# Performance work log

Hardware: AMD Instinct MI355X
Metric: run time of the kernel (lower is better)

Reference implementation:

```python
import jax, jax.numpy as jnp
import numpy as np

N, T, INPUT_DIM, HIDDEN_DIM = 8, 4096, 128, 128


def setup_inputs() -> dict:
    key = jax.random.key(0)
    k_h, k_wq, k_bq, k_wk, k_bk = jax.random.split(key, 5)
    s = 1.0 / np.sqrt(INPUT_DIM)
    return {
        "H": jax.random.normal(k_h, (N, T, INPUT_DIM), dtype=jnp.float32),
        "Wq": jax.random.uniform(k_wq, (INPUT_DIM, HIDDEN_DIM), jnp.float32, -s, s),
        "bq": jax.random.uniform(k_bq, (HIDDEN_DIM,), jnp.float32, -s, s),
        "Wk": jax.random.uniform(k_wk, (INPUT_DIM, HIDDEN_DIM), jnp.float32, -s, s),
        "bk": jax.random.uniform(k_bk, (HIDDEN_DIM,), jnp.float32, -s, s),
    }


def reference(H, Wq, bq, Wk, bk):
    # Q, K: [N, T, hidden]
    Q = jnp.einsum("ntd,dh->nth", H, Wq) + bq
    K = jnp.einsum("ntd,dh->nth", H, Wk) + bk
    # Faithful quirk: original scales by sqrt(K.transpose(-1,-2).size(-1)) == sqrt(T),
    # NOT sqrt(hidden_dim).
    T_ = H.shape[1]
    scale = 1.0 / jnp.sqrt(jnp.asarray(T_, dtype=H.dtype))
    A = jnp.einsum("nth,nsh->nts", Q, K) * scale  # [N, T, T]
    A = jax.nn.softmax(A, axis=-1)
    # Attention applied directly to H (no V projection), plus residual.
    return jnp.einsum("nts,nsd->ntd", A, H) + H
```

## Files before the change

### kernel.cpp

```cpp
#include <hip/hip_runtime.h>
#include <hip/hip_bf16.h>

typedef __attribute__((ext_vector_type(4))) float f32x4;
typedef __attribute__((ext_vector_type(16))) float f32x16;
typedef __attribute__((ext_vector_type(8))) short s16x8;
typedef unsigned int u32;

#define DEVINL static __device__ __forceinline__

constexpr int TDIM = 4096;
constexpr int DDIM = 128;
constexpr float QSCALE = 1.4426950408889634f / 64.0f;

DEVINL unsigned short f2bf(float f) {
  union { float f; unsigned u; } v; v.f = f;
  unsigned r = v.u + 0x7fffu + ((v.u >> 16) & 1u);
  return (unsigned short)(r >> 16);
}

__global__ void wtrans_kernel(const float* __restrict__ Wq,
                              const float* __restrict__ Wk,
                              unsigned short* __restrict__ Wtq,
                              unsigned short* __restrict__ Wtk) {
  const float* src = blockIdx.x ? Wk : Wq;
  unsigned short* dst = blockIdx.x ? Wtk : Wtq;
  int tid = threadIdx.x;
  for (int k = 0; k < 64; ++k) {
    int e = tid + k * 256;
    int h = e >> 7, d = e & 127;
    dst[h * 128 + d] = f2bf(src[d * 128 + h]);
  }
}

__global__ __launch_bounds__(256) void proj_kernel(
    const float* __restrict__ H, const float* __restrict__ bq,
    const float* __restrict__ bk, const unsigned short* __restrict__ Wtq,
    const unsigned short* __restrict__ Wtk, char* __restrict__ Qb,
    char* __restrict__ Kb, char* __restrict__ Vt) {
  __shared__ __align__(16) unsigned short hs[64][136];
  __shared__ __align__(16) char qs[16384];
  __shared__ __align__(16) char kt[16384];
  __shared__ __align__(16) char vt[16384];
  int b = blockIdx.x;
  int n = b >> 6;
  int t0 = (b & 63) << 6;
  int tid = threadIdx.x;
  const float* Hrow = H + (size_t)(n * TDIM + t0) * DDIM;
#pragma unroll
  for (int k = 0; k < 8; ++k) {
    int e = tid + k * 256;
    int r = e >> 5;
    int c = (e & 31) << 2;
    f32x4 v = *(const f32x4*)(Hrow + r * DDIM + c);
    unsigned short bf[4] = {f2bf(v.x), f2bf(v.y), f2bf(v.z), f2bf(v.w)};
    unsigned short* p = &hs[r][c];
    p[0] = bf[0]; p[1] = bf[1]; p[2] = bf[2]; p[3] = bf[3];
#pragma unroll
    for (int j = 0; j < 4; ++j) {
      int d = c + j;
      int byte = ((d >> 1) * 256 + (d & 1) * 128 + r * 2) ^
                 (((d >> 1) & 15) << 4);
      *(unsigned short*)(vt + byte) = bf[j];
    }
  }
  __syncthreads();
  int w = tid >> 6, ln = tid & 63;
  int lm = ln & 15, lg = ln >> 4;
  int m0 = w * 16;
  s16x8 af[4];
#pragma unroll
  for (int kf = 0; kf < 4; ++kf)
    af[kf] = *(const s16x8*)&hs[m0 + lm][kf * 32 + lg * 8];
#pragma unroll
  for (int nt = 0; nt < 8; ++nt) {
    f32x4 acc = {0.f, 0.f, 0.f, 0.f};
#pragma unroll
    for (int kf = 0; kf < 4; ++kf) {
      s16x8 bfr = *(const s16x8*)&Wtq[(nt * 16 + lm) * 128 + kf * 32 + lg * 8];
      acc = __builtin_amdgcn_mfma_f32_16x16x32_bf16(af[kf], bfr, acc, 0, 0, 0);
    }
    int h = nt * 16 + lm;
    float bv = bq[h];
#pragma unroll
    for (int i = 0; i < 4; ++i) {
      int tl = m0 + lg * 4 + i;
      int byte = tl * 256 + ((h * 2) ^ ((tl & 15) << 4));
      *(unsigned short*)(qs + byte) = f2bf((acc[i] + bv) * QSCALE);
    }
  }
#pragma unroll
  for (int nt = 0; nt < 8; ++nt) {
    f32x4 acc = {0.f, 0.f, 0.f, 0.f};
#pragma unroll
    for (int kf = 0; kf < 4; ++kf) {
      s16x8 bfr = *(const s16x8*)&Wtk[(nt * 16 + lm) * 128 + kf * 32 + lg * 8];
      acc = __builtin_amdgcn_mfma_f32_16x16x32_bf16(af[kf], bfr, acc, 0, 0, 0);
    }
    int hip2 = ((lm >> 3) & 1) * 32;
    int jj = lm & 7;
#pragma unroll
    for (int i = 0; i < 4; ++i) {
      int rl = m0 + lg * 4 + i;
      int byte = (rl >> 5) * 8192 + nt * 1024 + (hip2 + (rl & 31)) * 16 + jj * 2;
      *(unsigned short*)(kt + byte) = f2bf(acc[i] + bk[nt * 16 + lm]);
    }
  }
  __syncthreads();
  size_t base = (size_t)(n * TDIM + t0) * 256;
  size_t vbase = ((size_t)(n * 64 + (t0 >> 6)) << 14);
#pragma unroll
  for (int k = 0; k < 4; ++k) {
    int off = tid * 16 + k * 4096;
    *(f32x4*)(Qb + base + off) = *(const f32x4*)(qs + off);
    *(f32x4*)(Kb + base + off) = *(const f32x4*)(kt + off);
    *(f32x4*)(Vt + vbase + off) = *(const f32x4*)(vt + off);
  }
}

DEVINL void stage16(const char* g, char* s, int w, int ln) {
#pragma unroll
  for (int j = 0; j < 2; ++j) {
    int off = (w * 2 + j) * 1024;
    __builtin_amdgcn_global_load_lds(
        (const __attribute__((address_space(1))) void*)(g + off + ln * 16),
        (__attribute__((address_space(3))) void*)(s + off), 16, 0, 0);
  }
}

__global__ __launch_bounds__(512, 2) void attn_kernel(
    const char* __restrict__ Qsw, const char* __restrict__ Ksw,
    const char* __restrict__ Vsw, const float* __restrict__ H,
    float* __restrict__ Out) {
  __shared__ __align__(16) char lds[69632];
  int b = blockIdx.x;
  int n = b & 7;
  int q0 = (b >> 3) << 7;
  int tid = threadIdx.x;
  int w = tid >> 6, ln = tid & 63;
  int q32 = ln & 31, hi = ln >> 5;
  int ws = w & 3;
  int st = w >> 2;
  int qrow = q0 + ws * 32;
  int swz = (q32 & 15) << 4;
  int dpl = q32 >> 1;
  int vswz = dpl << 4;
  int dphalf = (q32 & 1) * 128;

  const char* Kn = Ksw + (size_t)n * (TDIM * 256);
  const char* Vn0 = Vsw + (size_t)n * (64 * 16384);
  const char* Vn1 = Vn0 + (size_t)32 * 16384;

  const char* Qn = Qsw + (size_t)(n * TDIM + qrow + q32) * 256;
  s16x8 qf[8];
#pragma unroll
  for (int d = 0; d < 8; ++d)
    qf[d] = *(const s16x8*)(Qn + ((d * 32 + hi * 16) ^ swz));

  f32x16 o[4];
#pragma unroll
  for (int dt = 0; dt < 4; ++dt) o[dt] = (f32x16)0.0f;
  float lsum = 0.f;

  stage16(Vn0, lds + 0, w, ln);
  stage16(Vn1, lds + 32768, w, ln);
  __syncthreads();

  for (int it = 0; it < 32; ++it) {
    int c = it & 1;
    if (it < 31) {
      int p2 = c ^ 1;
      size_t go = (size_t)(it + 1) * 16384;
      stage16(Vn0 + go, lds + p2 * 16384, w, ln);
      stage16(Vn1 + go, lds + 32768 + p2 * 16384, w, ln);
    }
    const char* vb = lds + st * 32768 + c * 16384;
    const char* kt = Kn + ((size_t)(st * 32 + it) << 14);

    f32x16 s0 = (f32x16)0.0f, s1 = (f32x16)0.0f;
#pragma unroll
    for (int d = 0; d < 8; ++d) {
      s16x8 ka0 = *(const s16x8*)(kt + d * 1024 + ln * 16);
      s16x8 ka1 = *(const s16x8*)(kt + 8192 + d * 1024 + ln * 16);
      s0 = __builtin_amdgcn_mfma_f32_32x32x16_bf16(ka0, qf[d], s0, 0, 0, 0);
      s1 = __builtin_amdgcn_mfma_f32_32x32x16_bf16(ka1, qf[d], s1, 0, 0, 0);
    }

    f32x16 p0, p1;
#pragma unroll
    for (int r = 0; r < 16; ++r) {
      p0[r] = __builtin_amdgcn_exp2f(s0[r]);
      p1[r] = __builtin_amdgcn_exp2f(s1[r]);
    }
    float ls = 0.f;
#pragma unroll
    for (int r = 0; r < 16; ++r) ls += p0[r] + p1[r];
    lsum += ls;

    s16x8 pa[4];
#pragma unroll
    for (int kt2 = 0; kt2 < 2; ++kt2) {
      u32 P2[8];
#pragma unroll
      for (int r = 0; r < 8; ++r) {
        float e0 = kt2 ? p1[2 * r] : p0[2 * r];
        float e1 = kt2 ? p1[2 * r + 1] : p0[2 * r + 1];
        asm("v_cvt_pk_bf16_f32 %0, %1, %2" : "=v"(P2[r]) : "v"(e0), "v"(e1));
      }
#pragma unroll
      for (int b2 = 0; b2 < 2; ++b2) {
        u32 a0 = P2[b2 * 4 + 0], c0 = P2[b2 * 4 + 2];
        u32 a1 = P2[b2 * 4 + 1], c1 = P2[b2 * 4 + 3];
        asm("v_permlane32_swap_b32 %0, %1" : "+v"(a0), "+v"(c0));
        asm("v_permlane32_swap_b32 %0, %1" : "+v"(a1), "+v"(c1));
        union { u32 u[4]; s16x8 v; } pk;
        pk.u[0] = a0; pk.u[1] = a1; pk.u[2] = c0; pk.u[3] = c1;
        pa[kt2 * 2 + b2] = pk.v;
      }
    }

    __builtin_amdgcn_s_setprio(1);
#pragma unroll
    for (int ks = 0; ks < 4; ++ks) {
      int colv = dphalf + ks * 32 + hi * 16;
#pragma unroll
      for (int dt = 0; dt < 4; ++dt) {
        int dp = dt * 16 + dpl;
        s16x8 vv = *(const s16x8*)(vb + ((dp * 256 + colv) ^ vswz));
        o[dt] = __builtin_amdgcn_mfma_f32_32x32x16_bf16(pa[ks], vv, o[dt], 0, 0, 0);
      }
    }
    __builtin_amdgcn_s_setprio(0);
    __syncthreads();
  }

  if (w >= 4) {
    char* dst = lds + (w - 4) * 16896;
#pragma unroll
    for (int dt = 0; dt < 4; ++dt)
#pragma unroll
      for (int c4 = 0; c4 < 4; ++c4) {
        f32x4 ch = {o[dt][c4 * 4 + 0], o[dt][c4 * 4 + 1],
                    o[dt][c4 * 4 + 2], o[dt][c4 * 4 + 3]};
        *(f32x4*)(dst + ((dt * 4 + c4) * 64 + ln) * 16) = ch;
      }
    *(float*)(dst + 16384 + ln * 4) = lsum;
  }
  __syncthreads();
  if (w < 4) {
    const char* src = lds + w * 16896;
#pragma unroll
    for (int dt = 0; dt < 4; ++dt)
#pragma unroll
      for (int c4 = 0; c4 < 4; ++c4) {
        f32x4 ch = *(const f32x4*)(src + ((dt * 4 + c4) * 64 + ln) * 16);
        o[dt][c4 * 4 + 0] += ch.x; o[dt][c4 * 4 + 1] += ch.y;
        o[dt][c4 * 4 + 2] += ch.z; o[dt][c4 * 4 + 3] += ch.w;
      }
    lsum += *(const float*)(src + 16384 + ln * 4);
    u32 la = __builtin_bit_cast(u32, lsum), lb = la;
    asm("v_permlane32_swap_b32 %0, %1" : "+v"(la), "+v"(lb));
    float ltot = __builtin_bit_cast(float, la) + __builtin_bit_cast(float, lb);
    float invl = 1.0f / ltot;
    if (hi == 0) *(float*)(lds + 67584 + w * 128 + q32 * 4) = invl;
  }
  __syncthreads();
  if (w < 4) {
    const float* Hn = H + (size_t)n * TDIM * DDIM;
    float* On = Out + (size_t)n * TDIM * DDIM;
    float iv[16];
#pragma unroll
    for (int r = 0; r < 16; ++r) {
      int qr = (r & 3) + 8 * (r >> 2) + 4 * hi;
      iv[r] = *(const float*)(lds + 67584 + w * 128 + qr * 4);
    }
#pragma unroll
    for (int dt = 0; dt < 4; ++dt)
#pragma unroll
      for (int r = 0; r < 16; ++r) {
        int qr = (r & 3) + 8 * (r >> 2) + 4 * hi;
        size_t idx = (size_t)(qrow + qr) * DDIM + dt * 32 + q32;
        On[idx] = o[dt][r] * iv[r] + Hn[idx];
      }
  }
}

extern "C" void kernel_launch(void* const* d_in, const int* in_sizes, int n_in,
                              void* d_out, int out_size, void* d_ws, size_t ws_size,
                              hipStream_t stream) {
  const float* H  = (const float*)d_in[0];
  const float* Wq = (const float*)d_in[1];
  const float* bq = (const float*)d_in[2];
  const float* Wk = (const float*)d_in[3];
  const float* bk = (const float*)d_in[4];
  float* Out = (float*)d_out;
  char* ws = (char*)d_ws;
  unsigned short* Wtq = (unsigned short*)(ws);
  unsigned short* Wtk = (unsigned short*)(ws + 32768);
  char* Qb = ws + 65536;
  char* Kb = ws + 65536 + 8388608;
  char* Vt = ws + 65536 + 2 * 8388608;

  wtrans_kernel<<<2, 256, 0, stream>>>(Wq, Wk, Wtq, Wtk);
  proj_kernel<<<512, 256, 0, stream>>>(H, bq, bk, Wtq, Wtk, Qb, Kb, Vt);
  attn_kernel<<<256, 512, 0, stream>>>(Qb, Kb, Vt, H, Out);
}
```

Measured before the change: 126.1 us.

## Fold Wk into query projection and reuse bf16 H as keys

Scores are rewritten as (H Wq Wk^T + bq Wk^T) H^T: a prep kernel forms M = Wq Wk^T and u = Wk bq, and the key projection is dropped, since the bk term is constant per row and cancels in softmax. The attention kernel then stages both K (the bf16 H itself) and V tiles into a larger double-buffered LDS. Each wave now computes 64 query rows against a quarter of the key range, sharing each K and V fragment across two MFMAs, and partial results are combined through an LDS tree reduction. This removes one projection GEMM and halves fragment loads per MFMA, at the cost of 128KB of LDS, which likely limits the kernel to one block per CU, and more register pressure.

```diff
diff --git a/kernel.cpp b/kernel.cpp
--- a/kernel.cpp
+++ b/kernel.cpp
@@ -18,24 +18,27 @@
   return (unsigned short)(r >> 16);
 }
 
-__global__ void wtrans_kernel(const float* __restrict__ Wq,
-                              const float* __restrict__ Wk,
-                              unsigned short* __restrict__ Wtq,
-                              unsigned short* __restrict__ Wtk) {
-  const float* src = blockIdx.x ? Wk : Wq;
-  unsigned short* dst = blockIdx.x ? Wtk : Wtq;
-  int tid = threadIdx.x;
-  for (int k = 0; k < 64; ++k) {
-    int e = tid + k * 256;
-    int h = e >> 7, d = e & 127;
-    dst[h * 128 + d] = f2bf(src[d * 128 + h]);
+__global__ __launch_bounds__(256) void prep_kernel(
+    const float* __restrict__ Wq, const float* __restrict__ Wk,
+    const float* __restrict__ bq, unsigned short* __restrict__ Mt,
+    float* __restrict__ u) {
+  int idx = blockIdx.x * 256 + threadIdx.x;
+  int e = idx >> 7, d = idx & 127;
+  float acc = 0.f;
+#pragma unroll 4
+  for (int h = 0; h < 128; ++h) acc += Wq[d * 128 + h] * Wk[e * 128 + h];
+  Mt[e * 128 + d] = f2bf(acc);
+  if (blockIdx.x == 0 && threadIdx.x < 128) {
+    float a = 0.f;
+#pragma unroll 4
+    for (int h = 0; h < 128; ++h) a += Wk[threadIdx.x * 128 + h] * bq[h];
+    u[threadIdx.x] = a;
   }
 }
 
 __global__ __launch_bounds__(256) void proj_kernel(
-    const float* __restrict__ H, const float* __restrict__ bq,
-    const float* __restrict__ bk, const unsigned short* __restrict__ Wtq,
-    const unsigned short* __restrict__ Wtk, char* __restrict__ Qb,
+    const float* __restrict__ H, const unsigned short* __restrict__ Mt,
+    const float* __restrict__ u, char* __restrict__ Qb,
     char* __restrict__ Kb, char* __restrict__ Vt) {
   __shared__ __align__(16) unsigned short hs[64][136];
   __shared__ __align__(16) char qs[16384];
@@ -55,11 +58,16 @@
     unsigned short bf[4] = {f2bf(v.x), f2bf(v.y), f2bf(v.z), f2bf(v.w)};
     unsigned short* p = &hs[r][c];
     p[0] = bf[0]; p[1] = bf[1]; p[2] = bf[2]; p[3] = bf[3];
+    int kbyte = r * 256 + ((c * 2) ^ ((r & 15) << 4));
+    unsigned short* kp = (unsigned short*)(kt + kbyte);
+    kp[0] = bf[0]; kp[1] = bf[1]; kp[2] = bf[2]; kp[3] = bf[3];
+    int p32 = r >> 5, tl = r & 31;
 #pragma unroll
     for (int j = 0; j < 4; ++j) {
       int d = c + j;
-      int byte = ((d >> 1) * 256 + (d & 1) * 128 + r * 2) ^
-                 (((d >> 1) & 15) << 4);
+      int dp = d >> 1, half = d & 1;
+      int byte = p32 * 8192 + dp * 128 +
+                 ((half * 64 + tl * 2) ^ ((dp & 7) << 4));
       *(unsigned short*)(vt + byte) = bf[j];
     }
   }
@@ -76,38 +84,21 @@
     f32x4 acc = {0.f, 0.f, 0.f, 0.f};
 #pragma unroll
     for (int kf = 0; kf < 4; ++kf) {
-      s16x8 bfr = *(const s16x8*)&Wtq[(nt * 16 + lm) * 128 + kf * 32 + lg * 8];
+      s16x8 bfr = *(const s16x8*)&Mt[(nt * 16 + lm) * 128 + kf * 32 + lg * 8];
       acc = __builtin_amdgcn_mfma_f32_16x16x32_bf16(af[kf], bfr, acc, 0, 0, 0);
     }
-    int h = nt * 16 + lm;
-    float bv = bq[h];
+    int e = nt * 16 + lm;
+    float bv = u[e];
 #pragma unroll
     for (int i = 0; i < 4; ++i) {
       int tl = m0 + lg * 4 + i;
-      int byte = tl * 256 + ((h * 2) ^ ((tl & 15) << 4));
+      int byte = tl * 256 + ((e * 2) ^ ((tl & 15) << 4));
       *(unsigned short*)(qs + byte) = f2bf((acc[i] + bv) * QSCALE);
     }
   }
-#pragma unroll
-  for (int nt = 0; nt < 8; ++nt) {
-    f32x4 acc = {0.f, 0.f, 0.f, 0.f};
-#pragma unroll
-    for (int kf = 0; kf < 4; ++kf) {
-      s16x8 bfr = *(const s16x8*)&Wtk[(nt * 16 + lm) * 128 + kf * 32 + lg * 8];
-      acc = __builtin_amdgcn_mfma_f32_16x16x32_bf16(af[kf], bfr, acc, 0, 0, 0);
-    }
-    int hip2 = ((lm >> 3) & 1) * 32;
-    int jj = lm & 7;
-#pragma unroll
-    for (int i = 0; i < 4; ++i) {
-      int rl = m0 + lg * 4 + i;
-      int byte = (rl >> 5) * 8192 + nt * 1024 + (hip2 + (rl & 31)) * 16 + jj * 2;
-      *(unsigned short*)(kt + byte) = f2bf(acc[i] + bk[nt * 16 + lm]);
-    }
-  }
   __syncthreads();
   size_t base = (size_t)(n * TDIM + t0) * 256;
-  size_t vbase = ((size_t)(n * 64 + (t0 >> 6)) << 14);
+  size_t vbase = (size_t)(n * 128 + (t0 >> 5)) * 8192;
 #pragma unroll
   for (int k = 0; k < 4; ++k) {
     int off = tid * 16 + k * 4096;
@@ -117,13 +108,12 @@
   }
 }
 
-DEVINL void stage16(const char* g, char* s, int w, int ln) {
-#pragma unroll
-  for (int j = 0; j < 2; ++j) {
-    int off = (w * 2 + j) * 1024;
+DEVINL void stage8(const char* g, char* s, int ln) {
+#pragma unroll
+  for (int j = 0; j < 8; ++j) {
     __builtin_amdgcn_global_load_lds(
-        (const __attribute__((address_space(1))) void*)(g + off + ln * 16),
-        (__attribute__((address_space(3))) void*)(s + off), 16, 0, 0);
+        (const __attribute__((address_space(1))) void*)(g + j * 1024 + ln * 16),
+        (__attribute__((address_space(3))) void*)(s + j * 1024), 16, 0, 0);
   }
 }
 
@@ -131,81 +121,82 @@
     const char* __restrict__ Qsw, const char* __restrict__ Ksw,
     const char* __restrict__ Vsw, const float* __restrict__ H,
     float* __restrict__ Out) {
-  __shared__ __align__(16) char lds[69632];
+  __shared__ __align__(16) char lds[131072];
   int b = blockIdx.x;
   int n = b & 7;
   int q0 = (b >> 3) << 7;
   int tid = threadIdx.x;
   int w = tid >> 6, ln = tid & 63;
   int q32 = ln & 31, hi = ln >> 5;
-  int ws = w & 3;
-  int st = w >> 2;
-  int qrow = q0 + ws * 32;
+  int qg = w >> 2;
+  int kvs = w & 3;
+  int qrow = q0 + qg * 64;
   int swz = (q32 & 15) << 4;
   int dpl = q32 >> 1;
-  int vswz = dpl << 4;
-  int dphalf = (q32 & 1) * 128;
+  int vcol = (q32 & 1) * 64;
 
   const char* Kn = Ksw + (size_t)n * (TDIM * 256);
-  const char* Vn0 = Vsw + (size_t)n * (64 * 16384);
-  const char* Vn1 = Vn0 + (size_t)32 * 16384;
-
-  const char* Qn = Qsw + (size_t)(n * TDIM + qrow + q32) * 256;
-  s16x8 qf[8];
-#pragma unroll
-  for (int d = 0; d < 8; ++d)
-    qf[d] = *(const s16x8*)(Qn + ((d * 32 + hi * 16) ^ swz));
-
-  f32x16 o[4];
-#pragma unroll
-  for (int dt = 0; dt < 4; ++dt) o[dt] = (f32x16)0.0f;
-  float lsum = 0.f;
-
-  stage16(Vn0, lds + 0, w, ln);
-  stage16(Vn1, lds + 32768, w, ln);
+  const char* Vn = Vsw + (size_t)n * (128 * 8192);
+
+  const char* Qlo = Qsw + (size_t)(n * TDIM + qrow + q32) * 256;
+  const char* Qhi = Qlo + 32 * 256;
+  s16x8 qfl[8], qfh[8];
+#pragma unroll
+  for (int d = 0; d < 8; ++d) {
+    int off = (d * 32 + hi * 16) ^ swz;
+    qfl[d] = *(const s16x8*)(Qlo + off);
+    qfh[d] = *(const s16x8*)(Qhi + off);
+  }
+
+  f32x16 o[8];
+#pragma unroll
+  for (int i = 0; i < 8; ++i) o[i] = (f32x16)0.0f;
+  float lsl = 0.f, lsh = 0.f;
+
+  int stp = w & 3, typ = w >> 2;
+  {
+    const char* g = typ ? (Vn + (size_t)(stp * 32) * 8192)
+                        : (Kn + (size_t)(stp * 1024) * 256);
+    stage8(g, lds + stp * 16384 + typ * 8192, ln);
+  }
   __syncthreads();
 
   for (int it = 0; it < 32; ++it) {
     int c = it & 1;
     if (it < 31) {
-      int p2 = c ^ 1;
-      size_t go = (size_t)(it + 1) * 16384;
-      stage16(Vn0 + go, lds + p2 * 16384, w, ln);
-      stage16(Vn1 + go, lds + 32768 + p2 * 16384, w, ln);
-    }
-    const char* vb = lds + st * 32768 + c * 16384;
-    const char* kt = Kn + ((size_t)(st * 32 + it) << 14);
-
-    f32x16 s0 = (f32x16)0.0f, s1 = (f32x16)0.0f;
+      int kvn = stp * 1024 + (it + 1) * 32;
+      const char* g = typ ? (Vn + (size_t)(kvn >> 5) * 8192)
+                          : (Kn + (size_t)kvn * 256);
+      stage8(g, lds + (c ^ 1) * 65536 + stp * 16384 + typ * 8192, ln);
+    }
+    const char* kb = lds + c * 65536 + kvs * 16384;
+    const char* vb = kb + 8192;
+
+    f32x16 sl = (f32x16)0.0f, sh = (f32x16)0.0f;
+    __builtin_amdgcn_s_setprio(1);
 #pragma unroll
     for (int d = 0; d < 8; ++d) {
-      s16x8 ka0 = *(const s16x8*)(kt + d * 1024 + ln * 16);
-      s16x8 ka1 = *(const s16x8*)(kt + 8192 + d * 1024 + ln * 16);
-      s0 = __builtin_amdgcn_mfma_f32_32x32x16_bf16(ka0, qf[d], s0, 0, 0, 0);
-      s1 = __builtin_amdgcn_mfma_f32_32x32x16_bf16(ka1, qf[d], s1, 0, 0, 0);
-    }
-
-    f32x16 p0, p1;
+      s16x8 ka = *(const s16x8*)(kb + (q32 * 256 + ((d * 32 + hi * 16) ^ swz)));
+      sl = __builtin_amdgcn_mfma_f32_32x32x16_bf16(ka, qfl[d], sl, 0, 0, 0);
+      sh = __builtin_amdgcn_mfma_f32_32x32x16_bf16(ka, qfh[d], sh, 0, 0, 0);
+    }
+    __builtin_amdgcn_s_setprio(0);
+
 #pragma unroll
     for (int r = 0; r < 16; ++r) {
-      p0[r] = __builtin_amdgcn_exp2f(s0[r]);
-      p1[r] = __builtin_amdgcn_exp2f(s1[r]);
-    }
-    float ls = 0.f;
-#pragma unroll
-    for (int r = 0; r < 16; ++r) ls += p0[r] + p1[r];
-    lsum += ls;
-
-    s16x8 pa[4];
-#pragma unroll
-    for (int kt2 = 0; kt2 < 2; ++kt2) {
+      sl[r] = __builtin_amdgcn_exp2f(sl[r]);
+      lsl += sl[r];
+      sh[r] = __builtin_amdgcn_exp2f(sh[r]);
+      lsh += sh[r];
+    }
+
+    s16x8 pal[2], pah[2];
+    {
       u32 P2[8];
 #pragma unroll
-      for (int r = 0; r < 8; ++r) {
-        float e0 = kt2 ? p1[2 * r] : p0[2 * r];
-        float e1 = kt2 ? p1[2 * r + 1] : p0[2 * r + 1];
-        asm("v_cvt_pk_bf16_f32 %0, %1, %2" : "=v"(P2[r]) : "v"(e0), "v"(e1));
-      }
+      for (int r = 0; r < 8; ++r)
+        asm("v_cvt_pk_bf16_f32 %0, %1, %2"
+            : "=v"(P2[r]) : "v"(sl[2 * r]), "v"(sl[2 * r + 1]));
 #pragma unroll
       for (int b2 = 0; b2 < 2; ++b2) {
         u32 a0 = P2[b2 * 4 + 0], c0 = P2[b2 * 4 + 2];
@@ -214,74 +205,96 @@
         asm("v_permlane32_swap_b32 %0, %1" : "+v"(a1), "+v"(c1));
         union { u32 u[4]; s16x8 v; } pk;
         pk.u[0] = a0; pk.u[1] = a1; pk.u[2] = c0; pk.u[3] = c1;
-        pa[kt2 * 2 + b2] = pk.v;
+        pal[b2] = pk.v;
+      }
+#pragma unroll
+      for (int r = 0; r < 8; ++r)
+        asm("v_cvt_pk_bf16_f32 %0, %1, %2"
+            : "=v"(P2[r]) : "v"(sh[2 * r]), "v"(sh[2 * r + 1]));
+#pragma unroll
+      for (int b2 = 0; b2 < 2; ++b2) {
+        u32 a0 = P2[b2 * 4 + 0], c0 = P2[b2 * 4 + 2];
+        u32 a1 = P2[b2 * 4 + 1], c1 = P2[b2 * 4 + 3];
+        asm("v_permlane32_swap_b32 %0, %1" : "+v"(a0), "+v"(c0));
+        asm("v_permlane32_swap_b32 %0, %1" : "+v"(a1), "+v"(c1));
+        union { u32 u[4]; s16x8 v; } pk;
+        pk.u[0] = a0; pk.u[1] = a1; pk.u[2] = c0; pk.u[3] = c1;
+        pah[b2] = pk.v;
       }
     }
 
     __builtin_amdgcn_s_setprio(1);
 #pragma unroll
-    for (int ks = 0; ks < 4; ++ks) {
-      int colv = dphalf + ks * 32 + hi * 16;
+    for (int ks = 0; ks < 2; ++ks) {
 #pragma unroll
       for (int dt = 0; dt < 4; ++dt) {
-        int dp = dt * 16 + dpl;
-        s16x8 vv = *(const s16x8*)(vb + ((dp * 256 + colv) ^ vswz));
-        o[dt] = __builtin_amdgcn_mfma_f32_32x32x16_bf16(pa[ks], vv, o[dt], 0, 0, 0);
+        s16x8 vv = *(const s16x8*)(vb + ((dt * 16 + dpl) * 128 +
+                        ((vcol + ks * 32 + hi * 16) ^ ((dpl & 7) << 4))));
+        o[dt] = __builtin_amdgcn_mfma_f32_32x32x16_bf16(pal[ks], vv, o[dt], 0, 0, 0);
+        o[4 + dt] = __builtin_amdgcn_mfma_f32_32x32x16_bf16(pah[ks], vv, o[4 + dt], 0, 0, 0);
       }
     }
     __builtin_amdgcn_s_setprio(0);
     __syncthreads();
   }
 
-  if (w >= 4) {
-    char* dst = lds + (w - 4) * 16896;
-#pragma unroll
-    for (int dt = 0; dt < 4; ++dt)
-#pragma unroll
-      for (int c4 = 0; c4 < 4; ++c4) {
-        f32x4 ch = {o[dt][c4 * 4 + 0], o[dt][c4 * 4 + 1],
-                    o[dt][c4 * 4 + 2], o[dt][c4 * 4 + 3]};
-        *(f32x4*)(dst + ((dt * 4 + c4) * 64 + ln) * 16) = ch;
-      }
-    *(float*)(dst + 16384 + ln * 4) = lsum;
-  }
-  __syncthreads();
-  if (w < 4) {
-    const char* src = lds + w * 16896;
-#pragma unroll
-    for (int dt = 0; dt < 4; ++dt)
-#pragma unroll
-      for (int c4 = 0; c4 < 4; ++c4) {
-        f32x4 ch = *(const f32x4*)(src + ((dt * 4 + c4) * 64 + ln) * 16);
-        o[dt][c4 * 4 + 0] += ch.x; o[dt][c4 * 4 + 1] += ch.y;
-        o[dt][c4 * 4 + 2] += ch.z; o[dt][c4 * 4 + 3] += ch.w;
-      }
-    lsum += *(const float*)(src + 16384 + ln * 4);
-    u32 la = __builtin_bit_cast(u32, lsum), lb = la;
-    asm("v_permlane32_swap_b32 %0, %1" : "+v"(la), "+v"(lb));
-    float ltot = __builtin_bit_cast(float, la) + __builtin_bit_cast(float, lb);
-    float invl = 1.0f / ltot;
-    if (hi == 0) *(float*)(lds + 67584 + w * 128 + q32 * 4) = invl;
-  }
-  __syncthreads();
-  if (w < 4) {
+#define DUMP_O(dst)                                                      \
+  {                                                                      \
+    char* _d = (dst);                                                    \
+    _Pragma("unroll") for (int i = 0; i < 8; ++i)                        \
+      _Pragma("unroll") for (int c4 = 0; c4 < 4; ++c4) {                 \
+        f32x4 ch = {o[i][c4 * 4 + 0], o[i][c4 * 4 + 1],                  \
+                    o[i][c4 * 4 + 2], o[i][c4 * 4 + 3]};                 \
+        *(f32x4*)(_d + ((i * 4 + c4) * 64 + ln) * 16) = ch;              \
+      }                                                                  \
+  }
+#define ADD_O(src)                                                       \
+  {                                                                      \
+    const char* _s = (src);                                              \
+    _Pragma("unroll") for (int i = 0; i < 8; ++i)                        \
+      _Pragma("unroll") for (int c4 = 0; c4 < 4; ++c4) {                 \
+        f32x4 ch = *(const f32x4*)(_s + ((i * 4 + c4) * 64 + ln) * 16);  \
+        o[i][c4 * 4 + 0] += ch.x; o[i][c4 * 4 + 1] += ch.y;              \
+        o[i][c4 * 4 + 2] += ch.z; o[i][c4 * 4 + 3] += ch.w;              \
+      }                                                                  \
+  }
+  if (kvs & 1) DUMP_O(lds + (qg * 2 + (kvs >> 1)) * 32768);
+  __syncthreads();
+  if (!(kvs & 1)) ADD_O(lds + (qg * 2 + (kvs >> 1)) * 32768);
+  __syncthreads();
+  if (kvs == 2) DUMP_O(lds + qg * 2 * 32768);
+  {
+    float* lt = (float*)(lds + (qg * 2 + 1) * 32768);
+    lt[((kvs * 2 + hi) * 32 + q32) * 2 + 0] = lsl;
+    lt[((kvs * 2 + hi) * 32 + q32) * 2 + 1] = lsh;
+  }
+  __syncthreads();
+  if (kvs == 0) {
+    ADD_O(lds + qg * 2 * 32768);
+    const float* lt = (const float*)(lds + (qg * 2 + 1) * 32768);
     const float* Hn = H + (size_t)n * TDIM * DDIM;
     float* On = Out + (size_t)n * TDIM * DDIM;
-    float iv[16];
 #pragma unroll
     for (int r = 0; r < 16; ++r) {
       int qr = (r & 3) + 8 * (r >> 2) + 4 * hi;
-      iv[r] = *(const float*)(lds + 67584 + w * 128 + qr * 4);
-    }
-#pragma unroll
-    for (int dt = 0; dt < 4; ++dt)
-#pragma unroll
-      for (int r = 0; r < 16; ++r) {
-        int qr = (r & 3) + 8 * (r >> 2) + 4 * hi;
-        size_t idx = (size_t)(qrow + qr) * DDIM + dt * 32 + q32;
-        On[idx] = o[dt][r] * iv[r] + Hn[idx];
-      }
-  }
+      float suml = 0.f, sumh = 0.f;
+#pragma unroll
+      for (int t8 = 0; t8 < 8; ++t8) {
+        suml += lt[(t8 * 32 + qr) * 2 + 0];
+        sumh += lt[(t8 * 32 + qr) * 2 + 1];
+      }
+      float il = 1.0f / suml, ih = 1.0f / sumh;
+#pragma unroll
+      for (int dt = 0; dt < 4; ++dt) {
+        size_t ilo = (size_t)(qrow + qr) * DDIM + dt * 32 + q32;
+        size_t ihi = (size_t)(qrow + 32 + qr) * DDIM + dt * 32 + q32;
+        On[ilo] = o[dt][r] * il + Hn[ilo];
+        On[ihi] = o[4 + dt][r] * ih + Hn[ihi];
+      }
+    }
+  }
+#undef DUMP_O
+#undef ADD_O
 }
 
 extern "C" void kernel_launch(void* const* d_in, const int* in_sizes, int n_in,
@@ -292,15 +305,16 @@
   const float* bq = (const float*)d_in[2];
   const float* Wk = (const float*)d_in[3];
   const float* bk = (const float*)d_in[4];
+  (void)bk;
   float* Out = (float*)d_out;
   char* ws = (char*)d_ws;
-  unsigned short* Wtq = (unsigned short*)(ws);
-  unsigned short* Wtk = (unsigned short*)(ws + 32768);
+  unsigned short* Mt = (unsigned short*)(ws);
+  float* u = (float*)(ws + 32768);
   char* Qb = ws + 65536;
   char* Kb = ws + 65536 + 8388608;
   char* Vt = ws + 65536 + 2 * 8388608;
 
-  wtrans_kernel<<<2, 256, 0, stream>>>(Wq, Wk, Wtq, Wtk);
-  proj_kernel<<<512, 256, 0, stream>>>(H, bq, bk, Wtq, Wtk, Qb, Kb, Vt);
+  prep_kernel<<<64, 256, 0, stream>>>(Wq, Wk, bq, Mt, u);
+  proj_kernel<<<512, 256, 0, stream>>>(H, Mt, u, Qb, Kb, Vt);
   attn_kernel<<<256, 512, 0, stream>>>(Qb, Kb, Vt, H, Out);
 }
```

Result: faster. 117.2 us (-7.1%).

## Fold Wq·Wkᵀ into one projection, split KV across blocks, merge partials

Applied to the files above, without the earlier changes.

Precomputes M = Wq·Wkᵀ and u = Wk·bq so that only one projection (H·M + u) is needed, and H itself serves as the key. This removes the K projection GEMM; the bk terms are constant per query row and cancel in the softmax. The attention kernel now stages both K and V tiles into LDS with 256-thread blocks and splits the KV range across two blocks instead of two wave groups. It writes partial outputs and row sums to workspace, and a new merge kernel combines them, normalises and adds the residual. The cost is extra global traffic for the partial outputs plus an additional kernel launch.

```diff
diff --git a/kernel.cpp b/kernel.cpp
--- a/kernel.cpp
+++ b/kernel.cpp
@@ -18,24 +18,27 @@
   return (unsigned short)(r >> 16);
 }
 
-__global__ void wtrans_kernel(const float* __restrict__ Wq,
-                              const float* __restrict__ Wk,
-                              unsigned short* __restrict__ Wtq,
-                              unsigned short* __restrict__ Wtk) {
-  const float* src = blockIdx.x ? Wk : Wq;
-  unsigned short* dst = blockIdx.x ? Wtk : Wtq;
-  int tid = threadIdx.x;
-  for (int k = 0; k < 64; ++k) {
-    int e = tid + k * 256;
-    int h = e >> 7, d = e & 127;
-    dst[h * 128 + d] = f2bf(src[d * 128 + h]);
+__global__ __launch_bounds__(256) void prep_kernel(
+    const float* __restrict__ Wq, const float* __restrict__ Wk,
+    const float* __restrict__ bq, unsigned short* __restrict__ Mt,
+    float* __restrict__ u) {
+  int idx = blockIdx.x * 256 + threadIdx.x;
+  int e = idx >> 7, d = idx & 127;
+  float acc = 0.f;
+#pragma unroll 4
+  for (int h = 0; h < 128; ++h) acc += Wq[d * 128 + h] * Wk[e * 128 + h];
+  Mt[e * 128 + d] = f2bf(acc);
+  if (blockIdx.x == 0 && threadIdx.x < 128) {
+    float a = 0.f;
+#pragma unroll 4
+    for (int h = 0; h < 128; ++h) a += Wk[threadIdx.x * 128 + h] * bq[h];
+    u[threadIdx.x] = a;
   }
 }
 
 __global__ __launch_bounds__(256) void proj_kernel(
-    const float* __restrict__ H, const float* __restrict__ bq,
-    const float* __restrict__ bk, const unsigned short* __restrict__ Wtq,
-    const unsigned short* __restrict__ Wtk, char* __restrict__ Qb,
+    const float* __restrict__ H, const unsigned short* __restrict__ Mt,
+    const float* __restrict__ u, char* __restrict__ Qb,
     char* __restrict__ Kb, char* __restrict__ Vt) {
   __shared__ __align__(16) unsigned short hs[64][136];
   __shared__ __align__(16) char qs[16384];
@@ -55,11 +58,14 @@
     unsigned short bf[4] = {f2bf(v.x), f2bf(v.y), f2bf(v.z), f2bf(v.w)};
     unsigned short* p = &hs[r][c];
     p[0] = bf[0]; p[1] = bf[1]; p[2] = bf[2]; p[3] = bf[3];
+    int kbyte = r * 256 + ((c * 2) ^ ((r & 15) << 4));
+    unsigned short* kp = (unsigned short*)(kt + kbyte);
+    kp[0] = bf[0]; kp[1] = bf[1]; kp[2] = bf[2]; kp[3] = bf[3];
 #pragma unroll
     for (int j = 0; j < 4; ++j) {
       int d = c + j;
-      int byte = ((d >> 1) * 256 + (d & 1) * 128 + r * 2) ^
-                 (((d >> 1) & 15) << 4);
+      int dp = d >> 1, half = d & 1;
+      int byte = dp * 256 + ((half * 128 + r * 2) ^ ((dp & 15) << 4));
       *(unsigned short*)(vt + byte) = bf[j];
     }
   }
@@ -76,33 +82,16 @@
     f32x4 acc = {0.f, 0.f, 0.f, 0.f};
 #pragma unroll
     for (int kf = 0; kf < 4; ++kf) {
-      s16x8 bfr = *(const s16x8*)&Wtq[(nt * 16 + lm) * 128 + kf * 32 + lg * 8];
+      s16x8 bfr = *(const s16x8*)&Mt[(nt * 16 + lm) * 128 + kf * 32 + lg * 8];
       acc = __builtin_amdgcn_mfma_f32_16x16x32_bf16(af[kf], bfr, acc, 0, 0, 0);
     }
-    int h = nt * 16 + lm;
-    float bv = bq[h];
+    int e = nt * 16 + lm;
+    float bv = u[e];
 #pragma unroll
     for (int i = 0; i < 4; ++i) {
       int tl = m0 + lg * 4 + i;
-      int byte = tl * 256 + ((h * 2) ^ ((tl & 15) << 4));
+      int byte = tl * 256 + ((e * 2) ^ ((tl & 15) << 4));
       *(unsigned short*)(qs + byte) = f2bf((acc[i] + bv) * QSCALE);
-    }
-  }
-#pragma unroll
-  for (int nt = 0; nt < 8; ++nt) {
-    f32x4 acc = {0.f, 0.f, 0.f, 0.f};
-#pragma unroll
-    for (int kf = 0; kf < 4; ++kf) {
-      s16x8 bfr = *(const s16x8*)&Wtk[(nt * 16 + lm) * 128 + kf * 32 + lg * 8];
-      acc = __builtin_amdgcn_mfma_f32_16x16x32_bf16(af[kf], bfr, acc, 0, 0, 0);
-    }
-    int hip2 = ((lm >> 3) & 1) * 32;
-    int jj = lm & 7;
-#pragma unroll
-    for (int i = 0; i < 4; ++i) {
-      int rl = m0 + lg * 4 + i;
-      int byte = (rl >> 5) * 8192 + nt * 1024 + (hip2 + (rl & 31)) * 16 + jj * 2;
-      *(unsigned short*)(kt + byte) = f2bf(acc[i] + bk[nt * 16 + lm]);
     }
   }
   __syncthreads();
@@ -117,38 +106,37 @@
   }
 }
 
-DEVINL void stage16(const char* g, char* s, int w, int ln) {
-#pragma unroll
-  for (int j = 0; j < 2; ++j) {
-    int off = (w * 2 + j) * 1024;
+DEVINL void stage8(const char* g, char* s, int ln) {
+#pragma unroll
+  for (int j = 0; j < 8; ++j) {
     __builtin_amdgcn_global_load_lds(
-        (const __attribute__((address_space(1))) void*)(g + off + ln * 16),
-        (__attribute__((address_space(3))) void*)(s + off), 16, 0, 0);
-  }
-}
-
-__global__ __launch_bounds__(512, 2) void attn_kernel(
+        (const __attribute__((address_space(1))) void*)(g + j * 1024 + ln * 16),
+        (__attribute__((address_space(3))) void*)(s + j * 1024), 16, 0, 0);
+  }
+}
+
+__global__ __launch_bounds__(256, 2) void attn_kernel(
     const char* __restrict__ Qsw, const char* __restrict__ Ksw,
-    const char* __restrict__ Vsw, const float* __restrict__ H,
-    float* __restrict__ Out) {
-  __shared__ __align__(16) char lds[69632];
+    const char* __restrict__ Vsw, float* __restrict__ Out,
+    float* __restrict__ Op1, float* __restrict__ Lp) {
+  __shared__ __align__(16) char kbuf[2][16384];
+  __shared__ __align__(16) char vbuf[2][16384];
   int b = blockIdx.x;
   int n = b & 7;
-  int q0 = (b >> 3) << 7;
+  int st = (b >> 3) & 1;
+  int q0 = (b >> 4) << 7;
   int tid = threadIdx.x;
   int w = tid >> 6, ln = tid & 63;
   int q32 = ln & 31, hi = ln >> 5;
-  int ws = w & 3;
-  int st = w >> 2;
-  int qrow = q0 + ws * 32;
+  int qrow = q0 + w * 32;
   int swz = (q32 & 15) << 4;
   int dpl = q32 >> 1;
   int vswz = dpl << 4;
   int dphalf = (q32 & 1) * 128;
 
   const char* Kn = Ksw + (size_t)n * (TDIM * 256);
-  const char* Vn0 = Vsw + (size_t)n * (64 * 16384);
-  const char* Vn1 = Vn0 + (size_t)32 * 16384;
+  const char* Vn = Vsw + (size_t)n * (64 * 16384);
+  int kv0 = st * 2048;
 
   const char* Qn = Qsw + (size_t)(n * TDIM + qrow + q32) * 256;
   s16x8 qf[8];
@@ -161,29 +149,39 @@
   for (int dt = 0; dt < 4; ++dt) o[dt] = (f32x16)0.0f;
   float lsum = 0.f;
 
-  stage16(Vn0, lds + 0, w, ln);
-  stage16(Vn1, lds + 32768, w, ln);
+  {
+    const char* g = (w < 2) ? (Kn + (size_t)kv0 * 256 + w * 8192)
+                            : (Vn + (size_t)(kv0 >> 6) * 16384 + (w - 2) * 8192);
+    char* dst = (w < 2) ? (kbuf[0] + w * 8192) : (vbuf[0] + (w - 2) * 8192);
+    stage8(g, dst, ln);
+  }
   __syncthreads();
 
   for (int it = 0; it < 32; ++it) {
     int c = it & 1;
     if (it < 31) {
-      int p2 = c ^ 1;
-      size_t go = (size_t)(it + 1) * 16384;
-      stage16(Vn0 + go, lds + p2 * 16384, w, ln);
-      stage16(Vn1 + go, lds + 32768 + p2 * 16384, w, ln);
-    }
-    const char* vb = lds + st * 32768 + c * 16384;
-    const char* kt = Kn + ((size_t)(st * 32 + it) << 14);
+      int kvn = kv0 + (it + 1) * 64;
+      const char* g = (w < 2)
+          ? (Kn + (size_t)kvn * 256 + w * 8192)
+          : (Vn + (size_t)(kvn >> 6) * 16384 + (w - 2) * 8192);
+      char* dst = (w < 2) ? (kbuf[c ^ 1] + w * 8192)
+                          : (vbuf[c ^ 1] + (w - 2) * 8192);
+      stage8(g, dst, ln);
+    }
+    const char* kb = kbuf[c];
+    const char* vb = vbuf[c];
 
     f32x16 s0 = (f32x16)0.0f, s1 = (f32x16)0.0f;
+    __builtin_amdgcn_s_setprio(1);
 #pragma unroll
     for (int d = 0; d < 8; ++d) {
-      s16x8 ka0 = *(const s16x8*)(kt + d * 1024 + ln * 16);
-      s16x8 ka1 = *(const s16x8*)(kt + 8192 + d * 1024 + ln * 16);
+      int col = d * 32 + hi * 16;
+      s16x8 ka0 = *(const s16x8*)(kb + ((q32 * 256 + col) ^ swz));
+      s16x8 ka1 = *(const s16x8*)(kb + (((q32 + 32) * 256 + col) ^ swz));
       s0 = __builtin_amdgcn_mfma_f32_32x32x16_bf16(ka0, qf[d], s0, 0, 0, 0);
       s1 = __builtin_amdgcn_mfma_f32_32x32x16_bf16(ka1, qf[d], s1, 0, 0, 0);
     }
+    __builtin_amdgcn_s_setprio(0);
 
     f32x16 p0, p1;
 #pragma unroll
@@ -233,54 +231,38 @@
     __syncthreads();
   }
 
-  if (w >= 4) {
-    char* dst = lds + (w - 4) * 16896;
+  float* Og = st ? Op1 : Out;
+#pragma unroll
+  for (int r = 0; r < 16; ++r) {
+    int qr = (r & 3) + 8 * (r >> 2) + 4 * hi;
+    size_t rowbase = (size_t)(n * TDIM + qrow + qr) * DDIM;
 #pragma unroll
     for (int dt = 0; dt < 4; ++dt)
-#pragma unroll
-      for (int c4 = 0; c4 < 4; ++c4) {
-        f32x4 ch = {o[dt][c4 * 4 + 0], o[dt][c4 * 4 + 1],
-                    o[dt][c4 * 4 + 2], o[dt][c4 * 4 + 3]};
-        *(f32x4*)(dst + ((dt * 4 + c4) * 64 + ln) * 16) = ch;
-      }
-    *(float*)(dst + 16384 + ln * 4) = lsum;
-  }
-  __syncthreads();
-  if (w < 4) {
-    const char* src = lds + w * 16896;
-#pragma unroll
-    for (int dt = 0; dt < 4; ++dt)
-#pragma unroll
-      for (int c4 = 0; c4 < 4; ++c4) {
-        f32x4 ch = *(const f32x4*)(src + ((dt * 4 + c4) * 64 + ln) * 16);
-        o[dt][c4 * 4 + 0] += ch.x; o[dt][c4 * 4 + 1] += ch.y;
-        o[dt][c4 * 4 + 2] += ch.z; o[dt][c4 * 4 + 3] += ch.w;
-      }
-    lsum += *(const float*)(src + 16384 + ln * 4);
-    u32 la = __builtin_bit_cast(u32, lsum), lb = la;
-    asm("v_permlane32_swap_b32 %0, %1" : "+v"(la), "+v"(lb));
-    float ltot = __builtin_bit_cast(float, la) + __builtin_bit_cast(float, lb);
-    float invl = 1.0f / ltot;
-    if (hi == 0) *(float*)(lds + 67584 + w * 128 + q32 * 4) = invl;
-  }
-  __syncthreads();
-  if (w < 4) {
-    const float* Hn = H + (size_t)n * TDIM * DDIM;
-    float* On = Out + (size_t)n * TDIM * DDIM;
-    float iv[16];
-#pragma unroll
-    for (int r = 0; r < 16; ++r) {
-      int qr = (r & 3) + 8 * (r >> 2) + 4 * hi;
-      iv[r] = *(const float*)(lds + 67584 + w * 128 + qr * 4);
-    }
-#pragma unroll
-    for (int dt = 0; dt < 4; ++dt)
-#pragma unroll
-      for (int r = 0; r < 16; ++r) {
-        int qr = (r & 3) + 8 * (r >> 2) + 4 * hi;
-        size_t idx = (size_t)(qrow + qr) * DDIM + dt * 32 + q32;
-        On[idx] = o[dt][r] * iv[r] + Hn[idx];
-      }
+      Og[rowbase + dt * 32 + q32] = o[dt][r];
+  }
+  Lp[(size_t)(n * TDIM + qrow + q32) * 4 + st * 2 + hi] = lsum;
+}
+
+__global__ __launch_bounds__(256) void merge_kernel(
+    float* __restrict__ Out, const float* __restrict__ Op1,
+    const float* __restrict__ Lp, const float* __restrict__ H) {
+  int tid = threadIdx.x;
+  int row = blockIdx.x * 32 + (tid >> 3);
+  int col = (tid & 7) * 16;
+  f32x4 lp = *(const f32x4*)(Lp + (size_t)row * 4);
+  float il = 1.0f / (lp.x + lp.y + lp.z + lp.w);
+  size_t base = (size_t)row * DDIM + col;
+#pragma unroll
+  for (int j = 0; j < 4; ++j) {
+    f32x4 a = *(const f32x4*)(Out + base + j * 4);
+    f32x4 b2 = *(const f32x4*)(Op1 + base + j * 4);
+    f32x4 h = *(const f32x4*)(H + base + j * 4);
+    f32x4 r;
+    r.x = (a.x + b2.x) * il + h.x;
+    r.y = (a.y + b2.y) * il + h.y;
+    r.z = (a.z + b2.z) * il + h.z;
+    r.w = (a.w + b2.w) * il + h.w;
+    *(f32x4*)(Out + base + j * 4) = r;
   }
 }
 
@@ -292,15 +274,19 @@
   const float* bq = (const float*)d_in[2];
   const float* Wk = (const float*)d_in[3];
   const float* bk = (const float*)d_in[4];
+  (void)bk;
   float* Out = (float*)d_out;
   char* ws = (char*)d_ws;
-  unsigned short* Wtq = (unsigned short*)(ws);
-  unsigned short* Wtk = (unsigned short*)(ws + 32768);
+  unsigned short* Mt = (unsigned short*)(ws);
+  float* u = (float*)(ws + 32768);
   char* Qb = ws + 65536;
-  char* Kb = ws + 65536 + 8388608;
-  char* Vt = ws + 65536 + 2 * 8388608;
-
-  wtrans_kernel<<<2, 256, 0, stream>>>(Wq, Wk, Wtq, Wtk);
-  proj_kernel<<<512, 256, 0, stream>>>(H, bq, bk, Wtq, Wtk, Qb, Kb, Vt);
-  attn_kernel<<<256, 512, 0, stream>>>(Qb, Kb, Vt, H, Out);
-}
+  char* Kb = Qb + 8388608;
+  char* Vt = Kb + 8388608;
+  float* Op1 = (float*)(Vt + 8388608);
+  float* Lp = (float*)((char*)Op1 + 16777216);
+
+  prep_kernel<<<64, 256, 0, stream>>>(Wq, Wk, bq, Mt, u);
+  proj_kernel<<<512, 256, 0, stream>>>(H, Mt, u, Qb, Kb, Vt);
+  attn_kernel<<<512, 256, 0, stream>>>(Qb, Kb, Vt, Out, Op1, Lp);
+  merge_kernel<<<1024, 256, 0, stream>>>(Out, Op1, Lp, H);
+}
```

Measured after the change: 113.7 us. 9.9% less time.
